# Kernel tuning notes

Measured on AMD Instinct MI355X. Metric: run time of the kernel, lower is better.

The kernel has to match this reference:

```python
import jax, jax.numpy as jnp
import numpy as np

# Problem constants (would come from parameter_group in the original module)
N_POS = 512      # number of scan positions
BATCH = 32       # diffraction patterns per batch
N_OPR = 4        # OPR (orthogonal probe relaxation) modes
N_MODES = 8      # incoherent probe modes
H_OBJ = W_OBJ = 1024
HP = WP = 256    # probe / patch size
N_SLICES = 4     # multislice object
WAVELENGTH = 1.24e-10   # m (10 keV X-rays)
PIXEL = 1.0e-8          # m object pixel size
DZ = 2.0e-6             # m slice spacing


def _as_complex(x):
    return jax.lax.complex(x[..., 0], x[..., 1])


def _angular_spectrum_tf():
    # Transfer function H(fx,fy) = exp(i*dz*kz), kz = 2*pi/lambda * sqrt(1-(l*fx)^2-(l*fy)^2)
    fy = np.fft.fftfreq(HP, d=PIXEL)
    fx = np.fft.fftfreq(WP, d=PIXEL)
    FY, FX = np.meshgrid(fy, fx, indexing='ij')
    arg = 1.0 - (WAVELENGTH * FX) ** 2 - (WAVELENGTH * FY) ** 2
    kz = 2.0 * np.pi / WAVELENGTH * np.sqrt(np.maximum(arg, 0.0))
    tf = np.exp(1j * DZ * kz) * (arg > 0)  # evanescent cutoff
    return jnp.asarray(tf, jnp.complex64)

_TF = _angular_spectrum_tf()


def setup_inputs() -> dict:
    key = jax.random.key(0)
    k1, k2, k3, k4, k5 = jax.random.split(key, 5)
    object_ri = jax.random.normal(k1, (N_SLICES, H_OBJ, W_OBJ, 2), jnp.float32) * 0.1
    # make object roughly a weak phase/amplitude modulator around 1
    object_ri = object_ri.at[..., 0].add(1.0)
    probe_ri = jax.random.normal(k2, (N_OPR, N_MODES, HP, WP, 2), jnp.float32)
    opr_weights = jax.random.normal(k3, (N_POS, N_OPR), jnp.float32) * 0.1
    opr_weights = opr_weights.at[:, 0].add(1.0)
    # positions (row, col) such that the 256x256 patch fits inside the object
    positions = jax.random.uniform(k4, (N_POS, 2), jnp.float32,
                                   minval=16.0, maxval=float(H_OBJ - HP - 16))
    indices = jax.random.randint(k5, (BATCH,), 0, N_POS, jnp.int32)
    return {"object_ri": object_ri, "probe_ri": probe_ri,
            "opr_weights": opr_weights, "positions": positions, "indices": indices}


def reference(object_ri, probe_ri, opr_weights, positions, indices):
    obj = _as_complex(object_ri)      # (S, H, W)
    probe = _as_complex(probe_ri)     # (K, M, h, w)
    pos = positions[indices]          # (B, 2)
    rpos = jnp.round(pos)
    frac = pos - rpos                 # fractional shifts compensated on probe
    ipos = rpos.astype(jnp.int32)

    # --- gather object patches at rounded positions: (B, S, h, w) ---
    def get_patch(rc):
        return jax.lax.dynamic_slice(obj, (0, rc[0], rc[1]), (N_SLICES, HP, WP))
    patches = jax.vmap(get_patch)(ipos)

    # --- unique probes via OPR weighting of mode 0 ---
    w = opr_weights[indices].astype(probe.dtype)           # (B, K)
    p0 = jnp.einsum('bk,khw->bhw', w, probe[:, 0])         # (B, h, w)
    pk = jnp.broadcast_to(probe[0, 1:], (pos.shape[0], N_MODES - 1, HP, WP))
    uprobe = jnp.concatenate([p0[:, None], pk], axis=1)    # (B, M, h, w)

    # --- subpixel Fourier shift of probes by fractional positions ---
    fy = jnp.fft.fftfreq(HP).astype(jnp.float32)
    fx = jnp.fft.fftfreq(WP).astype(jnp.float32)
    ramp = frac[:, 0, None, None] * fy[:, None] + frac[:, 1, None, None] * fx[None, :]
    phase = jnp.exp(jax.lax.complex(jnp.zeros_like(ramp), -2.0 * jnp.pi * ramp))  # (B, h, w)
    uprobe = jnp.fft.ifft2(jnp.fft.fft2(uprobe) * phase[:, None])

    # --- multislice propagation through the object ---
    psi = uprobe
    for s in range(N_SLICES):
        psi = patches[:, s, None] * psi                    # modulate
        if s < N_SLICES - 1:
            psi = jnp.fft.ifft2(jnp.fft.fft2(psi) * _TF)   # angular spectrum

    # --- far-field (Fourier) propagation to detector ---
    psi_far = jnp.fft.fftshift(
        jnp.fft.fft2(jnp.fft.ifftshift(psi, axes=(-2, -1)), norm='ortho'),
        axes=(-2, -1))
    # incoherent sum over probe modes -> detector intensities (B, h, w)
    return jnp.sum(jnp.abs(psi_far) ** 2, axis=1)
```

## Files before the change

kernel.cpp:

```cpp
#include <hip/hip_runtime.h>
#include <math.h>

#define HP 256
#define NB 32
#define NM 8
#define NK 4
#define NS 4
#define HOBJ 1024

__device__ __forceinline__ float2 cmul(float2 a, float2 b) {
    return make_float2(fmaf(a.x, b.x, -a.y * b.y), fmaf(a.x, b.y, a.y * b.x));
}

__constant__ float COS16[10] = {1.f, 0.9238795325f, 0.7071067812f, 0.3826834324f, 0.f,
                                -0.3826834324f, -0.7071067812f, -0.9238795325f, -1.f, -0.9238795325f};
__constant__ float SIN16[10] = {0.f, 0.3826834324f, 0.7071067812f, 0.9238795325f, 1.f,
                                0.9238795325f, 0.7071067812f, 0.3826834324f, 0.f, -0.3826834324f};

template <int S>
__device__ __forceinline__ void dft4(float2 a, float2 b, float2 c, float2 d,
                                     float2* o0, float2* o1, float2* o2, float2* o3) {
    float2 apc = make_float2(a.x + c.x, a.y + c.y);
    float2 amc = make_float2(a.x - c.x, a.y - c.y);
    float2 bpd = make_float2(b.x + d.x, b.y + d.y);
    float2 bmd = make_float2(b.x - d.x, b.y - d.y);
    float2 ib = (S < 0) ? make_float2(bmd.y, -bmd.x) : make_float2(-bmd.y, bmd.x);
    *o0 = make_float2(apc.x + bpd.x, apc.y + bpd.y);
    *o1 = make_float2(amc.x + ib.x, amc.y + ib.y);
    *o2 = make_float2(apc.x - bpd.x, apc.y - bpd.y);
    *o3 = make_float2(amc.x - ib.x, amc.y - ib.y);
}

template <int S>
__device__ __forceinline__ void fft16(float2 v[16]) {
    float2 t[16];
#pragma unroll
    for (int b = 0; b < 4; ++b)
        dft4<S>(v[b], v[4 + b], v[8 + b], v[12 + b],
                &t[4 * b + 0], &t[4 * b + 1], &t[4 * b + 2], &t[4 * b + 3]);
#pragma unroll
    for (int b = 1; b < 4; ++b)
#pragma unroll
        for (int c = 1; c < 4; ++c) {
            int j = b * c;
            float2 w = make_float2(COS16[j], (S < 0) ? -SIN16[j] : SIN16[j]);
            t[4 * b + c] = cmul(t[4 * b + c], w);
        }
#pragma unroll
    for (int c = 0; c < 4; ++c)
        dft4<S>(t[c], t[4 + c], t[8 + c], t[12 + c],
                &v[c + 0], &v[c + 4], &v[c + 8], &v[c + 12]);
}

template <int S, bool BS>
__device__ __forceinline__ void fft256(float2 v[16], int t, float* ldsRe, float* ldsIm) {
    fft16<S>(v);
    float sn, cs;
    __sincosf((float)S * 0.0245436926f  * (float)t, &sn, &cs);
    float2 base = make_float2(cs, sn);
    float2 cur = base;
#pragma unroll
    for (int k = 1; k < 16; ++k) {
        v[k] = cmul(v[k], cur);
        cur = cmul(cur, base);
    }
    if constexpr (BS) __syncthreads(); else asm volatile("" ::: "memory");
#pragma unroll
    for (int k = 0; k < 16; ++k) {
        ldsRe[k * 17 + t] = v[k].x;
        ldsIm[k * 17 + t] = v[k].y;
    }
    if constexpr (BS) __syncthreads(); else asm volatile("" ::: "memory");
#pragma unroll
    for (int j = 0; j < 16; ++j) {
        v[j].x = ldsRe[t * 17 + j];
        v[j].y = ldsIm[t * 17 + j];
    }
    fft16<S>(v);
}

#define ROWSTRIDE 272
#define COLSTRIDE 290

__global__ void k_init_shared(const float* __restrict__ probe, float2* __restrict__ sharedK) {
    __shared__ float sRe[16 * ROWSTRIDE], sIm[16 * ROWSTRIDE];
    int tt = threadIdx.x;
    int t = tt & 15, g = tt >> 4;
    int rowg = blockIdx.x, m = blockIdx.y + 1;
    int y = rowg * 16 + g;
    const float2* p = (const float2*)probe + (size_t)m * 65536 + (size_t)y * 256;
    float2 v[16];
#pragma unroll
    for (int n1 = 0; n1 < 16; ++n1) v[n1] = p[n1 * 16 + t];
    fft256<-1, false>(v, t, &sRe[g * ROWSTRIDE], &sIm[g * ROWSTRIDE]);
    float2* ob = sharedK + (size_t)(m - 1) * 65536 + (size_t)y * 256;
#pragma unroll
    for (int k2 = 0; k2 < 16; ++k2) ob[k2 * 16 + t] = v[k2];
}

__global__ void k_init_m0(const float* __restrict__ probe, const float* __restrict__ opr_w,
                          const int* __restrict__ indices, float2* __restrict__ buf, int b0) {
    __shared__ float sRe[16 * ROWSTRIDE], sIm[16 * ROWSTRIDE];
    int tt = threadIdx.x;
    int t = tt & 15, g = tt >> 4;
    int rowg = blockIdx.x, bl = blockIdx.z;
    int b = b0 + bl;
    int y = rowg * 16 + g;
    int idx = indices[b];
    float w0 = opr_w[idx * 4 + 0], w1 = opr_w[idx * 4 + 1];
    float w2 = opr_w[idx * 4 + 2], w3 = opr_w[idx * 4 + 3];
    const float2* p = (const float2*)probe;
    size_t rb = (size_t)y * 256;
    float2 v[16];
#pragma unroll
    for (int n1 = 0; n1 < 16; ++n1) {
        size_t o = rb + n1 * 16 + t;
        float2 p0 = p[o];
        float2 p1 = p[(size_t)(1 * NM) * 65536 + o];
        float2 p2 = p[(size_t)(2 * NM) * 65536 + o];
        float2 p3 = p[(size_t)(3 * NM) * 65536 + o];
        v[n1] = make_float2(w0 * p0.x + w1 * p1.x + w2 * p2.x + w3 * p3.x,
                            w0 * p0.y + w1 * p1.y + w2 * p2.y + w3 * p3.y);
    }
    fft256<-1, false>(v, t, &sRe[g * ROWSTRIDE], &sIm[g * ROWSTRIDE]);
    float2* ob = buf + (size_t)(bl * NM) * 65536 + (size_t)y * 256;
#pragma unroll
    for (int k2 = 0; k2 < 16; ++k2) ob[k2 * 16 + t] = v[k2];
}

__global__ void k_col_shift(const float* __restrict__ positions, const int* __restrict__ indices,
                            const float2* __restrict__ sharedK, float2* __restrict__ buf, int b0) {
    __shared__ float sRe[16 * COLSTRIDE], sIm[16 * COLSTRIDE];
    int tt = threadIdx.x;
    int c = tt & 15, t = tt >> 4;
    int colg = blockIdx.x, m = blockIdx.y, bl = blockIdx.z;
    int b = b0 + bl;
    int x = colg * 16 + c;
    int idx = indices[b];
    float py = positions[idx * 2 + 0], px = positions[idx * 2 + 1];
    float fr0 = py - rintf(py), fr1 = px - rintf(px);
    const float2* src = m ? (sharedK + (size_t)(m - 1) * 65536)
                          : (buf + (size_t)(bl * NM) * 65536);
    float2* dst = buf + (size_t)(bl * NM + m) * 65536;
    float2 v[16];
#pragma unroll
    for (int n1 = 0; n1 < 16; ++n1) v[n1] = src[(size_t)(n1 * 16 + t) * 256 + x];
    fft256<-1, true>(v, t, &sRe[c * COLSTRIDE], &sIm[c * COLSTRIDE]);
    float fxv = (float)((x < 128) ? x : x - 256) * (1.0f / 256.0f);
    float fy0 = (float)t * (1.0f / 256.0f);
    float sn, cs;
    __sincosf(-6.2831853071795864769f * (fr0 * fy0 + fr1 * fxv), &sn, &cs);
    float2 cur = make_float2(cs, sn);
    __sincosf(-6.2831853071795864769f * fr0 * (1.0f / 16.0f), &sn, &cs);
    float2 step = make_float2(cs, sn);
    __sincosf(6.2831853071795864769f * fr0, &sn, &cs);
    float2 wrap = make_float2(cs, sn);
#pragma unroll
    for (int k2 = 0; k2 < 16; ++k2) {
        if (k2 == 8) cur = cmul(cur, wrap);
        v[k2] = cmul(v[k2], cur);
        cur = cmul(cur, step);
    }
    fft256<1, true>(v, t, &sRe[c * COLSTRIDE], &sIm[c * COLSTRIDE]);
#pragma unroll
    for (int j = 0; j < 16; ++j) {
        float2 r = make_float2(v[j].x * (1.0f / 256.0f), v[j].y * (1.0f / 256.0f));
        dst[(size_t)(j * 16 + t) * 256 + x] = r;
    }
}

__global__ void k_row_prop(const float* __restrict__ object, const float* __restrict__ positions,
                           const int* __restrict__ indices, float2* __restrict__ buf, int b0, int s) {
    __shared__ float sRe[16 * ROWSTRIDE], sIm[16 * ROWSTRIDE];
    int tt = threadIdx.x;
    int t = tt & 15, g = tt >> 4;
    int rowg = blockIdx.x, m = blockIdx.y, bl = blockIdx.z;
    int b = b0 + bl;
    int y = rowg * 16 + g;
    int idx = indices[b];
    int r0 = (int)rintf(positions[idx * 2 + 0]);
    int r1 = (int)rintf(positions[idx * 2 + 1]);
    float2* img = buf + (size_t)(bl * NM + m) * 65536 + (size_t)y * 256;
    float2 v[16];
#pragma unroll
    for (int n1 = 0; n1 < 16; ++n1) v[n1] = img[n1 * 16 + t];
    fft256<1, false>(v, t, &sRe[g * ROWSTRIDE], &sIm[g * ROWSTRIDE]);
    const float2* obj = (const float2*)object + (size_t)s * HOBJ * HOBJ + (size_t)(r0 + y) * HOBJ + r1;
#pragma unroll
    for (int j = 0; j < 16; ++j) {
        int xx = t + 16 * j;
        float2 pz = obj[xx];
        float2 ps = make_float2(v[j].x * (1.0f / 256.0f), v[j].y * (1.0f / 256.0f));
        v[j] = cmul(ps, pz);
    }
    fft256<-1, false>(v, t, &sRe[g * ROWSTRIDE], &sIm[g * ROWSTRIDE]);
#pragma unroll
    for (int k2 = 0; k2 < 16; ++k2) img[k2 * 16 + t] = v[k2];
}

__global__ void k_col_tf(const float2* __restrict__ tf, float2* __restrict__ buf) {
    __shared__ float sRe[16 * COLSTRIDE], sIm[16 * COLSTRIDE];
    int tt = threadIdx.x;
    int c = tt & 15, t = tt >> 4;
    int colg = blockIdx.x, m = blockIdx.y, bl = blockIdx.z;
    int x = colg * 16 + c;
    float2* img = buf + (size_t)(bl * NM + m) * 65536;
    float2 v[16];
#pragma unroll
    for (int n1 = 0; n1 < 16; ++n1) v[n1] = img[(size_t)(n1 * 16 + t) * 256 + x];
    fft256<-1, true>(v, t, &sRe[c * COLSTRIDE], &sIm[c * COLSTRIDE]);
#pragma unroll
    for (int k2 = 0; k2 < 16; ++k2) {
        int ky = t + 16 * k2;
        v[k2] = cmul(v[k2], tf[ky * 256 + x]);
    }
    fft256<1, true>(v, t, &sRe[c * COLSTRIDE], &sIm[c * COLSTRIDE]);
#pragma unroll
    for (int j = 0; j < 16; ++j) {
        float2 r = make_float2(v[j].x * (1.0f / 256.0f), v[j].y * (1.0f / 256.0f));
        img[(size_t)(j * 16 + t) * 256 + x] = r;
    }
}

__global__ void k_col_final(const float2* __restrict__ buf, float* __restrict__ out, int b0) {
    __shared__ float sRe[16 * COLSTRIDE], sIm[16 * COLSTRIDE];
    int tt = threadIdx.x;
    int c = tt & 15, t = tt >> 4;
    int colg = blockIdx.x, bl = blockIdx.z;
    int x = colg * 16 + c;
    float acc[16];
#pragma unroll
    for (int j = 0; j < 16; ++j) acc[j] = 0.f;
    for (int m = 0; m < NM; ++m) {
        const float2* img = buf + (size_t)(bl * NM + m) * 65536;
        float2 v[16];
#pragma unroll
        for (int n1 = 0; n1 < 16; ++n1) v[n1] = img[(size_t)(n1 * 16 + t) * 256 + x];
        fft256<-1, true>(v, t, &sRe[c * COLSTRIDE], &sIm[c * COLSTRIDE]);
#pragma unroll
        for (int k2 = 0; k2 < 16; ++k2)
            acc[k2] = fmaf(v[k2].x, v[k2].x, fmaf(v[k2].y, v[k2].y, acc[k2]));
    }
    int b = b0 + bl;
    float* ob = out + (size_t)b * 65536;
    int xs = (x + 128) & 255;
#pragma unroll
    for (int k2 = 0; k2 < 16; ++k2) {
        int ky = t + 16 * k2;
        int ys = (ky + 128) & 255;
        ob[ys * 256 + xs] = acc[k2] * (1.0f / 65536.0f);
    }
}

__global__ void k_tf(float2* __restrict__ tf) {
    int i = blockIdx.x * 256 + threadIdx.x;
    int ky = i >> 8, kx = i & 255;
    double fy = (double)((ky < 128) ? ky : ky - 256) / (256.0 * 1.0e-8);
    double fx = (double)((kx < 128) ? kx : kx - 256) / (256.0 * 1.0e-8);
    double ly = 1.24e-10 * fy, lx = 1.24e-10 * fx;
    double arg = 1.0 - lx * lx - ly * ly;
    float2 r = make_float2(0.f, 0.f);
    if (arg > 0.0) {
        double kz = (2.0 * M_PI / 1.24e-10) * sqrt(arg);
        double ph = 2.0e-6 * kz;
        r = make_float2((float)cos(ph), (float)sin(ph));
    }
    tf[i] = r;
}

extern "C" void kernel_launch(void* const* d_in, const int* in_sizes, int n_in,
                              void* d_out, int out_size, void* d_ws, size_t ws_size,
                              hipStream_t stream) {
    const float* object = (const float*)d_in[0];
    const float* probe = (const float*)d_in[1];
    const float* opr_w = (const float*)d_in[2];
    const float* positions = (const float*)d_in[3];
    const int* indices = (const int*)d_in[4];
    float* out = (float*)d_out;

    float2* tf = (float2*)d_ws;
    float2* sharedK = (float2*)((char*)d_ws + ((size_t)1 << 20));
    float2* buf = (float2*)((char*)d_ws + ((size_t)8 << 20));
    size_t head = (size_t)8 << 20;
    size_t avail = (ws_size > head) ? ws_size - head : 0;
    long long perb = (long long)NM * 65536 * sizeof(float2);
    int Bc = (int)(avail / perb);
    if (Bc > NB) Bc = NB;
    if (Bc < 1) Bc = 1;

    k_tf<<<256, 256, 0, stream>>>(tf);
    k_init_shared<<<dim3(16, NM - 1, 1), 256, 0, stream>>>(probe, sharedK);

    for (int b0 = 0; b0 < NB; b0 += Bc) {
        int bc = (NB - b0 < Bc) ? (NB - b0) : Bc;
        dim3 grid(16, NM, bc);
        k_init_m0<<<dim3(16, 1, bc), 256, 0, stream>>>(probe, opr_w, indices, buf, b0);
        k_col_shift<<<grid, 256, 0, stream>>>(positions, indices, sharedK, buf, b0);
        for (int s = 0; s < NS; ++s) {
            k_row_prop<<<grid, 256, 0, stream>>>(object, positions, indices, buf, b0, s);
            if (s < NS - 1) k_col_tf<<<grid, 256, 0, stream>>>(tf, buf);
        }
        dim3 gridE(16, 1, bc);
        k_col_final<<<gridE, 256, 0, stream>>>(buf, out, b0);
    }
}
```

Measured before the change: 486.7 us.

## Halve LDS transpose scratch and split final mode reduction across blocks with atomics

The FFT transpose now goes through one shared buffer, moving the real and imaginary parts in two passes instead of keeping separate Re and Im arrays. This halves LDS per block, which should allow more resident blocks, but adds extra barriers and LDS round trips. Separately, the final far-field kernel splits the 8 modes into 4 blocks of 2 modes each and accumulates into a pre-zeroed output with float atomics. This raises parallelism in the final stage at the cost of a zeroing kernel, atomic traffic and a summation order that is no longer deterministic.

```diff
diff --git a/kernel.cpp b/kernel.cpp
--- a/kernel.cpp
+++ b/kernel.cpp
@@ -10,6 +10,10 @@
 
 __device__ __forceinline__ float2 cmul(float2 a, float2 b) {
     return make_float2(fmaf(a.x, b.x, -a.y * b.y), fmaf(a.x, b.y, a.y * b.x));
+}
+
+__device__ __forceinline__ void atomAddF(float* p, float v) {
+    __hip_atomic_fetch_add(p, v, __ATOMIC_RELAXED, __HIP_MEMORY_SCOPE_AGENT);
 }
 
 __constant__ float COS16[10] = {1.f, 0.9238795325f, 0.7071067812f, 0.3826834324f, 0.f,
@@ -53,7 +57,7 @@
 }
 
 template <int S, bool BS>
-__device__ __forceinline__ void fft256(float2 v[16], int t, float* ldsRe, float* ldsIm) {
+__device__ __forceinline__ void fft256(float2 v[16], int t, float* lds) {
     fft16<S>(v);
     float sn, cs;
     __sincosf((float)S * 0.0245436926f  * (float)t, &sn, &cs);
@@ -66,16 +70,16 @@
     }
     if constexpr (BS) __syncthreads(); else asm volatile("" ::: "memory");
 #pragma unroll
-    for (int k = 0; k < 16; ++k) {
-        ldsRe[k * 17 + t] = v[k].x;
-        ldsIm[k * 17 + t] = v[k].y;
-    }
+    for (int k = 0; k < 16; ++k) lds[k * 17 + t] = v[k].x;
     if constexpr (BS) __syncthreads(); else asm volatile("" ::: "memory");
 #pragma unroll
-    for (int j = 0; j < 16; ++j) {
-        v[j].x = ldsRe[t * 17 + j];
-        v[j].y = ldsIm[t * 17 + j];
-    }
+    for (int j = 0; j < 16; ++j) v[j].x = lds[t * 17 + j];
+    if constexpr (BS) __syncthreads(); else asm volatile("" ::: "memory");
+#pragma unroll
+    for (int k = 0; k < 16; ++k) lds[k * 17 + t] = v[k].y;
+    if constexpr (BS) __syncthreads(); else asm volatile("" ::: "memory");
+#pragma unroll
+    for (int j = 0; j < 16; ++j) v[j].y = lds[t * 17 + j];
     fft16<S>(v);
 }
 
@@ -83,7 +87,7 @@
 #define COLSTRIDE 290
 
 __global__ void k_init_shared(const float* __restrict__ probe, float2* __restrict__ sharedK) {
-    __shared__ float sRe[16 * ROWSTRIDE], sIm[16 * ROWSTRIDE];
+    __shared__ float sc[16 * ROWSTRIDE];
     int tt = threadIdx.x;
     int t = tt & 15, g = tt >> 4;
     int rowg = blockIdx.x, m = blockIdx.y + 1;
@@ -92,7 +96,7 @@
     float2 v[16];
 #pragma unroll
     for (int n1 = 0; n1 < 16; ++n1) v[n1] = p[n1 * 16 + t];
-    fft256<-1, false>(v, t, &sRe[g * ROWSTRIDE], &sIm[g * ROWSTRIDE]);
+    fft256<-1, false>(v, t, &sc[g * ROWSTRIDE]);
     float2* ob = sharedK + (size_t)(m - 1) * 65536 + (size_t)y * 256;
 #pragma unroll
     for (int k2 = 0; k2 < 16; ++k2) ob[k2 * 16 + t] = v[k2];
@@ -100,7 +104,7 @@
 
 __global__ void k_init_m0(const float* __restrict__ probe, const float* __restrict__ opr_w,
                           const int* __restrict__ indices, float2* __restrict__ buf, int b0) {
-    __shared__ float sRe[16 * ROWSTRIDE], sIm[16 * ROWSTRIDE];
+    __shared__ float sc[16 * ROWSTRIDE];
     int tt = threadIdx.x;
     int t = tt & 15, g = tt >> 4;
     int rowg = blockIdx.x, bl = blockIdx.z;
@@ -122,7 +126,7 @@
         v[n1] = make_float2(w0 * p0.x + w1 * p1.x + w2 * p2.x + w3 * p3.x,
                             w0 * p0.y + w1 * p1.y + w2 * p2.y + w3 * p3.y);
     }
-    fft256<-1, false>(v, t, &sRe[g * ROWSTRIDE], &sIm[g * ROWSTRIDE]);
+    fft256<-1, false>(v, t, &sc[g * ROWSTRIDE]);
     float2* ob = buf + (size_t)(bl * NM) * 65536 + (size_t)y * 256;
 #pragma unroll
     for (int k2 = 0; k2 < 16; ++k2) ob[k2 * 16 + t] = v[k2];
@@ -130,7 +134,7 @@
 
 __global__ void k_col_shift(const float* __restrict__ positions, const int* __restrict__ indices,
                             const float2* __restrict__ sharedK, float2* __restrict__ buf, int b0) {
-    __shared__ float sRe[16 * COLSTRIDE], sIm[16 * COLSTRIDE];
+    __shared__ float sc[16 * COLSTRIDE];
     int tt = threadIdx.x;
     int c = tt & 15, t = tt >> 4;
     int colg = blockIdx.x, m = blockIdx.y, bl = blockIdx.z;
@@ -145,7 +149,7 @@
     float2 v[16];
 #pragma unroll
     for (int n1 = 0; n1 < 16; ++n1) v[n1] = src[(size_t)(n1 * 16 + t) * 256 + x];
-    fft256<-1, true>(v, t, &sRe[c * COLSTRIDE], &sIm[c * COLSTRIDE]);
+    fft256<-1, true>(v, t, &sc[c * COLSTRIDE]);
     float fxv = (float)((x < 128) ? x : x - 256) * (1.0f / 256.0f);
     float fy0 = (float)t * (1.0f / 256.0f);
     float sn, cs;
@@ -161,7 +165,7 @@
         v[k2] = cmul(v[k2], cur);
         cur = cmul(cur, step);
     }
-    fft256<1, true>(v, t, &sRe[c * COLSTRIDE], &sIm[c * COLSTRIDE]);
+    fft256<1, true>(v, t, &sc[c * COLSTRIDE]);
 #pragma unroll
     for (int j = 0; j < 16; ++j) {
         float2 r = make_float2(v[j].x * (1.0f / 256.0f), v[j].y * (1.0f / 256.0f));
@@ -171,7 +175,7 @@
 
 __global__ void k_row_prop(const float* __restrict__ object, const float* __restrict__ positions,
                            const int* __restrict__ indices, float2* __restrict__ buf, int b0, int s) {
-    __shared__ float sRe[16 * ROWSTRIDE], sIm[16 * ROWSTRIDE];
+    __shared__ float sc[16 * ROWSTRIDE];
     int tt = threadIdx.x;
     int t = tt & 15, g = tt >> 4;
     int rowg = blockIdx.x, m = blockIdx.y, bl = blockIdx.z;
@@ -184,7 +188,7 @@
     float2 v[16];
 #pragma unroll
     for (int n1 = 0; n1 < 16; ++n1) v[n1] = img[n1 * 16 + t];
-    fft256<1, false>(v, t, &sRe[g * ROWSTRIDE], &sIm[g * ROWSTRIDE]);
+    fft256<1, false>(v, t, &sc[g * ROWSTRIDE]);
     const float2* obj = (const float2*)object + (size_t)s * HOBJ * HOBJ + (size_t)(r0 + y) * HOBJ + r1;
 #pragma unroll
     for (int j = 0; j < 16; ++j) {
@@ -193,13 +197,13 @@
         float2 ps = make_float2(v[j].x * (1.0f / 256.0f), v[j].y * (1.0f / 256.0f));
         v[j] = cmul(ps, pz);
     }
-    fft256<-1, false>(v, t, &sRe[g * ROWSTRIDE], &sIm[g * ROWSTRIDE]);
+    fft256<-1, false>(v, t, &sc[g * ROWSTRIDE]);
 #pragma unroll
     for (int k2 = 0; k2 < 16; ++k2) img[k2 * 16 + t] = v[k2];
 }
 
 __global__ void k_col_tf(const float2* __restrict__ tf, float2* __restrict__ buf) {
-    __shared__ float sRe[16 * COLSTRIDE], sIm[16 * COLSTRIDE];
+    __shared__ float sc[16 * COLSTRIDE];
     int tt = threadIdx.x;
     int c = tt & 15, t = tt >> 4;
     int colg = blockIdx.x, m = blockIdx.y, bl = blockIdx.z;
@@ -208,13 +212,13 @@
     float2 v[16];
 #pragma unroll
     for (int n1 = 0; n1 < 16; ++n1) v[n1] = img[(size_t)(n1 * 16 + t) * 256 + x];
-    fft256<-1, true>(v, t, &sRe[c * COLSTRIDE], &sIm[c * COLSTRIDE]);
+    fft256<-1, true>(v, t, &sc[c * COLSTRIDE]);
 #pragma unroll
     for (int k2 = 0; k2 < 16; ++k2) {
         int ky = t + 16 * k2;
         v[k2] = cmul(v[k2], tf[ky * 256 + x]);
     }
-    fft256<1, true>(v, t, &sRe[c * COLSTRIDE], &sIm[c * COLSTRIDE]);
+    fft256<1, true>(v, t, &sc[c * COLSTRIDE]);
 #pragma unroll
     for (int j = 0; j < 16; ++j) {
         float2 r = make_float2(v[j].x * (1.0f / 256.0f), v[j].y * (1.0f / 256.0f));
@@ -222,21 +226,28 @@
     }
 }
 
+__global__ void k_zero(float* __restrict__ out) {
+    int i = blockIdx.x * 256 + threadIdx.x;
+    ((float4*)out)[i] = make_float4(0.f, 0.f, 0.f, 0.f);
+}
+
 __global__ void k_col_final(const float2* __restrict__ buf, float* __restrict__ out, int b0) {
-    __shared__ float sRe[16 * COLSTRIDE], sIm[16 * COLSTRIDE];
+    __shared__ float sc[16 * COLSTRIDE];
     int tt = threadIdx.x;
     int c = tt & 15, t = tt >> 4;
-    int colg = blockIdx.x, bl = blockIdx.z;
+    int colg = blockIdx.x, mp = blockIdx.y, bl = blockIdx.z;
     int x = colg * 16 + c;
     float acc[16];
 #pragma unroll
     for (int j = 0; j < 16; ++j) acc[j] = 0.f;
-    for (int m = 0; m < NM; ++m) {
+#pragma unroll
+    for (int mi = 0; mi < 2; ++mi) {
+        int m = mp * 2 + mi;
         const float2* img = buf + (size_t)(bl * NM + m) * 65536;
         float2 v[16];
 #pragma unroll
         for (int n1 = 0; n1 < 16; ++n1) v[n1] = img[(size_t)(n1 * 16 + t) * 256 + x];
-        fft256<-1, true>(v, t, &sRe[c * COLSTRIDE], &sIm[c * COLSTRIDE]);
+        fft256<-1, true>(v, t, &sc[c * COLSTRIDE]);
 #pragma unroll
         for (int k2 = 0; k2 < 16; ++k2)
             acc[k2] = fmaf(v[k2].x, v[k2].x, fmaf(v[k2].y, v[k2].y, acc[k2]));
@@ -248,7 +259,7 @@
     for (int k2 = 0; k2 < 16; ++k2) {
         int ky = t + 16 * k2;
         int ys = (ky + 128) & 255;
-        ob[ys * 256 + xs] = acc[k2] * (1.0f / 65536.0f);
+        atomAddF(&ob[ys * 256 + xs], acc[k2] * (1.0f / 65536.0f));
     }
 }
 
@@ -290,6 +301,7 @@
 
     k_tf<<<256, 256, 0, stream>>>(tf);
     k_init_shared<<<dim3(16, NM - 1, 1), 256, 0, stream>>>(probe, sharedK);
+    k_zero<<<(NB * 65536) / (256 * 4), 256, 0, stream>>>(out);
 
     for (int b0 = 0; b0 < NB; b0 += Bc) {
         int bc = (NB - b0 < Bc) ? (NB - b0) : Bc;
@@ -300,7 +312,7 @@
             k_row_prop<<<grid, 256, 0, stream>>>(object, positions, indices, buf, b0, s);
             if (s < NS - 1) k_col_tf<<<grid, 256, 0, stream>>>(tf, buf);
         }
-        dim3 gridE(16, 1, bc);
+        dim3 gridE(16, 4, bc);
         k_col_final<<<gridE, 256, 0, stream>>>(buf, out, b0);
     }
 }
```

After: 513.5 us. 1.05x slower.
